# Kernel tuning notes

Measured on AMD Instinct MI355X. Metric: run time of the kernel, lower is better.

## Reference

```python
import jax, jax.numpy as jnp
import numpy as np

EPS = 1e-5  # InstanceNorm2d default eps


def setup_inputs() -> dict:
    key = jax.random.key(0)
    ks = jax.random.split(key, 6)
    B, S, C, KV, H = 4, 4096, 512, 960, 4
    emb = jax.random.normal(ks[0], (B, S, C), dtype=jnp.float32)
    emb_all = jax.random.normal(ks[1], (B, S, KV), dtype=jnp.float32)
    # nn.Linear weights are [out, in]; stacked per-head.
    Wq = jax.random.normal(ks[2], (H, C, C), dtype=jnp.float32) * 0.02
    Wk = jax.random.normal(ks[3], (H, KV, KV), dtype=jnp.float32) * 0.02
    Wv = jax.random.normal(ks[4], (H, KV, KV), dtype=jnp.float32) * 0.02
    Wo = jax.random.normal(ks[5], (C, C), dtype=jnp.float32) * 0.02
    return {"emb": emb, "emb_all": emb_all, "Wq": Wq, "Wk": Wk, "Wv": Wv, "Wo": Wo}


def reference(emb, emb_all, Wq, Wk, Wv, Wo):
    # Per-head linear projections (torch Linear: y = x @ W.T), batched over heads.
    Q = jnp.einsum('bsc,hdc->bhsd', emb, Wq)       # [B,H,S,C]
    K = jnp.einsum('bsk,hjk->bhsj', emb_all, Wk)   # [B,H,S,KV]
    V = jnp.einsum('bsk,hjk->bhsj', emb_all, Wv)   # [B,H,S,KV]
    kv_size = K.shape[-1]
    # Q is transposed(-1,-2) -> [B,H,C,S]; scores = Q^T @ K -> [B,H,C,KV]
    scores = jnp.einsum('bhsc,bhsk->bhck', Q, K) / jnp.sqrt(jnp.float32(kv_size))
    # InstanceNorm2d(num_heads): normalize each (b,h) plane over (C, KV), biased var, no affine.
    mean = jnp.mean(scores, axis=(2, 3), keepdims=True)
    var = jnp.var(scores, axis=(2, 3), keepdims=True)
    normed = (scores - mean) * jax.lax.rsqrt(var + EPS)
    probs = jax.nn.softmax(normed, axis=3)  # softmax over KV; dropout is identity (eval)
    # context = probs @ V^T -> [B,H,C,S]
    context = jnp.einsum('bhck,bhsk->bhcs', probs, V)
    # permute(0,3,2,1) -> [B,S,C,H], mean over heads -> [B,S,C]
    ctx = jnp.mean(context, axis=1).transpose(0, 2, 1)  # [B,S,C]
    out = jnp.einsum('bsc,dc->bsd', ctx, Wo)  # output Linear, no bias; proj dropout identity
    return out
```

## Files before the change

### kernel.cpp

```cpp
#include <hip/hip_runtime.h>
#include <math.h>

typedef __attribute__((ext_vector_type(8))) short short8;
typedef __attribute__((ext_vector_type(4))) float f32x4;

__device__ __forceinline__ unsigned short f2bf(float f) {
    unsigned int u; __builtin_memcpy(&u, &f, 4);
    unsigned int r = (u + 0x7FFFu + ((u >> 16) & 1u)) >> 16;
    return (unsigned short)r;
}
__device__ __forceinline__ float bf2f(unsigned short h) {
    unsigned int u = ((unsigned int)h) << 16;
    float f; __builtin_memcpy(&f, &u, 4); return f;
}
__device__ __forceinline__ void gl2lds16(const unsigned short* g, unsigned short* l) {
    __builtin_amdgcn_global_load_lds(
        (const __attribute__((address_space(1))) unsigned int*)g,
        (__attribute__((address_space(3))) unsigned int*)l, 16, 0, 0);
}

template<typename OutT, bool STATS>
__global__ __launch_bounds__(512)
void gemm_bt(const unsigned short* __restrict__ A, const unsigned short* __restrict__ B,
             OutT* __restrict__ C, float2* __restrict__ sp_out,
             int K, long lda, long ldb, long ldc,
             long sa_bb, long sa_bh, long sb_bb, long sb_bh, long sc_z,
             int H, float alpha)
{
    __shared__ unsigned short As[2][128 * 32];
    __shared__ unsigned short Bs[2][128 * 32];

    const int z = blockIdx.z;
    const int bb = z / H, hh = z - bb * H;
    A += (long)bb * sa_bb + (long)hh * sa_bh;
    B += (long)bb * sb_bb + (long)hh * sb_bh;
    C += (long)z * sc_z;

    const int tid  = threadIdx.x;
    const int lane = tid & 63;
    const int wave = tid >> 6;
    const int wr = wave >> 2, wc = wave & 3;

    const long m0 = (long)blockIdx.y * 128;
    const long n0 = (long)blockIdx.x * 128;

    const int lrow = lane >> 2;
    const int lcol = (lane & 3) * 8;
    const unsigned short* ga = A + (m0 + wave * 16 + lrow) * lda + lcol;
    const unsigned short* gb = B + (n0 + wave * 16 + lrow) * ldb + lcol;

    auto stg = [&](int buf, long koff) {
        gl2lds16(ga + koff, &As[buf][wave * 512]);
        gl2lds16(gb + koff, &Bs[buf][wave * 512]);
    };

    const int fr = lane & 15;
    const int fk = (lane >> 4) * 8;

    f32x4 acc[4][2];
    const f32x4 zero4 = {0.f, 0.f, 0.f, 0.f};
    #pragma unroll
    for (int i = 0; i < 4; ++i)
        #pragma unroll
        for (int j = 0; j < 2; ++j) acc[i][j] = zero4;

    stg(0, 0);
    stg(1, 32);

    int cur = 0;
    for (long k0 = 0; k0 < K; k0 += 32) {
        const bool ahead = (k0 + 64 < K);
        if (ahead) {
            asm volatile("s_waitcnt vmcnt(2)" ::: "memory");
        } else {
            asm volatile("s_waitcnt vmcnt(0)" ::: "memory");
        }
        __builtin_amdgcn_s_barrier();

        const unsigned short* ra = &As[cur][(wr * 64 + fr) * 32 + fk];
        const unsigned short* rb = &Bs[cur][(wc * 32 + fr) * 32 + fk];
        short8 af[4], bfr[2];
        #pragma unroll
        for (int i = 0; i < 4; ++i) af[i]  = *(const short8*)(ra + i * 512);
        #pragma unroll
        for (int j = 0; j < 2; ++j) bfr[j] = *(const short8*)(rb + j * 512);
        #pragma unroll
        for (int i = 0; i < 4; ++i)
            #pragma unroll
            for (int j = 0; j < 2; ++j)
                acc[i][j] = __builtin_amdgcn_mfma_f32_16x16x32_bf16(af[i], bfr[j], acc[i][j], 0, 0, 0);

        asm volatile("s_waitcnt lgkmcnt(0)" ::: "memory");
        __builtin_amdgcn_s_barrier();
        if (ahead) stg(cur, k0 + 64);
        cur ^= 1;
    }

    float s = 0.f, s2 = 0.f;
    const int orow = (lane >> 4) * 4;
    #pragma unroll
    for (int i = 0; i < 4; ++i) {
        const long rbase = m0 + wr * 64 + i * 16 + orow;
        #pragma unroll
        for (int j = 0; j < 2; ++j) {
            const long cidx = n0 + wc * 32 + j * 16 + fr;
            f32x4 v = acc[i][j];
            #pragma unroll
            for (int q = 0; q < 4; ++q) {
                float val = alpha * v[q];
                if constexpr (STATS) { s += val; s2 += val * val; }
                if constexpr (sizeof(OutT) == 4) C[(rbase + q) * ldc + cidx] = val;
                else                             C[(rbase + q) * ldc + cidx] = f2bf(val);
            }
        }
    }

    if constexpr (STATS) {
        float* red = (float*)&As[0][0];
        red[tid] = s; red[512 + tid] = s2;
        __syncthreads();
        for (int off = 256; off > 0; off >>= 1) {
            if (tid < off) { red[tid] += red[tid + off]; red[512 + tid] += red[512 + tid + off]; }
            __syncthreads();
        }
        if (tid == 0)
            sp_out[(long)z * 32 + blockIdx.y * gridDim.x + blockIdx.x] =
                make_float2(red[0], red[512]);
    }
}

__device__ __forceinline__
void tc64_impl(const float* __restrict__ in, unsigned short* __restrict__ outT,
               unsigned short* __restrict__ outB, int R, int Cin, long ldaT,
               int bx, int by, bool dual, unsigned short (*t)[68])
{
    const int r0 = bx * 64, c0 = by * 64;
    const int tid = threadIdx.x;
    const int rr  = tid >> 4;
    const int cc4 = (tid & 15) * 4;
    const bool real = (c0 + cc4) < Cin;

    #pragma unroll
    for (int i = 0; i < 4; ++i) {
        const int r = rr + i * 16;
        float4 v = make_float4(0.f, 0.f, 0.f, 0.f);
        if (real) v = *(const float4*)(in + (long)(r0 + r) * Cin + c0 + cc4);
        ushort4 o;
        o.x = f2bf(v.x); o.y = f2bf(v.y); o.z = f2bf(v.z); o.w = f2bf(v.w);
        *(ushort4*)&t[r][cc4] = o;
        if (dual && real)
            *(ushort4*)(outB + (long)(r0 + r) * Cin + c0 + cc4) = o;
    }
    __syncthreads();
    #pragma unroll
    for (int i = 0; i < 2; ++i) {
        const int p = rr + i * 16;
        const int c = 2 * p;
        ushort2 a0 = *(const ushort2*)&t[cc4 + 0][c];
        ushort2 a1 = *(const ushort2*)&t[cc4 + 1][c];
        ushort2 a2 = *(const ushort2*)&t[cc4 + 2][c];
        ushort2 a3 = *(const ushort2*)&t[cc4 + 3][c];
        ushort4 w0; w0.x = a0.x; w0.y = a1.x; w0.z = a2.x; w0.w = a3.x;
        ushort4 w1; w1.x = a0.y; w1.y = a1.y; w1.z = a2.y; w1.w = a3.y;
        *(ushort4*)(outT + (long)(c0 + c) * ldaT + r0 + cc4)     = w0;
        *(ushort4*)(outT + (long)(c0 + c + 1) * ldaT + r0 + cc4) = w1;
    }
}

__global__ __launch_bounds__(256)
void prep_all(const float* __restrict__ emb, const float* __restrict__ emb_all,
              const float* __restrict__ Wq, const float* __restrict__ Wk,
              const float* __restrict__ Wv, const float* __restrict__ Wo,
              unsigned short* __restrict__ embT, unsigned short* __restrict__ emb_allT,
              unsigned short* __restrict__ emb_allB, unsigned short* __restrict__ WqB,
              unsigned short* __restrict__ WkB, unsigned short* __restrict__ WvT,
              unsigned short* __restrict__ WoB)
{
    __shared__ unsigned short t[64][68];
    int bid = blockIdx.x;
    if (bid < 4096) {
        const int z = bid >> 10, r2 = bid & 1023, by = r2 >> 6, bx = r2 & 63;
        tc64_impl(emb_all + (long)z * 4096 * 960, emb_allT + (long)z * 1024 * 4096,
                  emb_allB + (long)z * 4096 * 960, 4096, 960, 4096, bx, by, true, t);
        return;
    }
    bid -= 4096;
    if (bid < 2048) {
        const int z = bid >> 9, r2 = bid & 511, by = r2 >> 6, bx = r2 & 63;
        tc64_impl(emb + (long)z * 4096 * 512, embT + (long)z * 512 * 4096,
                  nullptr, 4096, 512, 4096, bx, by, false, t);
        return;
    }
    bid -= 2048;
    if (bid < 960) {
        const int z = bid / 240, r2 = bid % 240, by = r2 / 15, bx = r2 % 15;
        tc64_impl(Wv + (long)z * 960 * 960, WvT + (long)z * 1024 * 960,
                  nullptr, 960, 960, 960, bx, by, false, t);
        return;
    }
    bid -= 960;
    long q = (long)bid * 256 + threadIdx.x;
    if (q < 983040) {
        long e = q * 4;
        long h = e / 983040L; long r2 = e - h * 983040L;
        long r = r2 / 960;    long c = r2 - r * 960;
        ushort4 o = {0, 0, 0, 0};
        if (r < 960) {
            float4 v = *(const float4*)(Wk + (h * 960 + r) * 960 + c);
            o.x = f2bf(v.x); o.y = f2bf(v.y); o.z = f2bf(v.z); o.w = f2bf(v.w);
        }
        *(ushort4*)(WkB + e) = o;
        return;
    }
    q -= 983040;
    if (q < 262144) {
        long e = q * 4;
        float4 v = *(const float4*)(Wq + e);
        ushort4 o; o.x = f2bf(v.x); o.y = f2bf(v.y); o.z = f2bf(v.z); o.w = f2bf(v.w);
        *(ushort4*)(WqB + e) = o;
        return;
    }
    q -= 262144;
    if (q < 65536) {
        long e = q * 4;
        float4 v = *(const float4*)(Wo + e);
        ushort4 o; o.x = f2bf(v.x); o.y = f2bf(v.y); o.z = f2bf(v.z); o.w = f2bf(v.w);
        *(ushort4*)(WoB + e) = o;
    }
}

__global__ __launch_bounds__(256)
void reduce_gt(const unsigned short* __restrict__ part, unsigned short* __restrict__ GT)
{
    long i = ((long)blockIdx.x * 256 + threadIdx.x) * 8;
    long b = i >> 19, r = i & 524287;
    const unsigned short* p = part + b * 4 * 524288 + r;
    const short8 v0 = *(const short8*)(p);
    const short8 v1 = *(const short8*)(p + 524288);
    const short8 v2 = *(const short8*)(p + 2 * 524288);
    const short8 v3 = *(const short8*)(p + 3 * 524288);
    short8 o;
    #pragma unroll
    for (int k = 0; k < 8; ++k) {
        float s = bf2f((unsigned short)v0[k]) + bf2f((unsigned short)v1[k])
                + bf2f((unsigned short)v2[k]) + bf2f((unsigned short)v3[k]);
        o[k] = (short)f2bf(s);
    }
    *(short8*)(GT + i) = o;
}

__global__ __launch_bounds__(256)
void norm_softmax(const unsigned short* __restrict__ SC, const float2* __restrict__ part,
                  unsigned short* __restrict__ probs)
{
    const int lane = threadIdx.x & 63;
    const int wave = threadIdx.x >> 6;
    const long row = (long)blockIdx.x * 4 + wave;
    const int z = (int)(row >> 9);

    float2 pv = part[z * 32 + (lane & 31)];
    float a = pv.x, b = pv.y;
    #pragma unroll
    for (int off = 1; off < 32; off <<= 1) {
        a += __shfl_xor(a, off);
        b += __shfl_xor(b, off);
    }
    const float ninv = 1.f / (512.f * 960.f);
    const float mean = a * ninv;
    const float rstd = rsqrtf(b * ninv - mean * mean + 960.f * 1e-5f);

    const unsigned short* p = SC + row * 1024 + lane * 16;
    const bool act = lane < 60;
    float x[16];
    {
        const short8 w0 = *(const short8*)(p);
        const short8 w1 = *(const short8*)(p + 8);
        #pragma unroll
        for (int k = 0; k < 8; ++k) {
            x[k]     = (bf2f((unsigned short)w0[k]) - mean) * rstd;
            x[k + 8] = (bf2f((unsigned short)w1[k]) - mean) * rstd;
        }
    }
    float mx = -1e30f;
    if (act) {
        #pragma unroll
        for (int k = 0; k < 16; ++k) mx = fmaxf(mx, x[k]);
    }
    #pragma unroll
    for (int off = 1; off < 64; off <<= 1) mx = fmaxf(mx, __shfl_xor(mx, off));

    float s = 0.f;
    if (act) {
        #pragma unroll
        for (int k = 0; k < 16; ++k) { x[k] = __expf(x[k] - mx); s += x[k]; }
    }
    #pragma unroll
    for (int off = 1; off < 64; off <<= 1) s += __shfl_xor(s, off);
    const float inv = 1.f / s;

    unsigned short* o = probs + row * 1024 + lane * 16;
    short8 o0 = {0,0,0,0,0,0,0,0}, o1 = {0,0,0,0,0,0,0,0};
    if (act) {
        #pragma unroll
        for (int k = 0; k < 8; ++k) {
            o0[k] = (short)f2bf(x[k] * inv);
            o1[k] = (short)f2bf(x[k + 8] * inv);
        }
    }
    *(short8*)(o)     = o0;
    *(short8*)(o + 8) = o1;
}

__global__ __launch_bounds__(256)
void mean_heads(const unsigned short* __restrict__ UT, unsigned short* __restrict__ Ub)
{
    const long per = 1024L * 512;
    long e = ((long)blockIdx.x * 256 + threadIdx.x) * 8;
    long b = e / per; long r = e - b * per;
    const short8 v0 = *(const short8*)(UT + (b * 4 + 0) * per + r);
    const short8 v1 = *(const short8*)(UT + (b * 4 + 1) * per + r);
    const short8 v2 = *(const short8*)(UT + (b * 4 + 2) * per + r);
    const short8 v3 = *(const short8*)(UT + (b * 4 + 3) * per + r);
    short8 o;
    #pragma unroll
    for (int k = 0; k < 8; ++k) {
        float s = bf2f((unsigned short)v0[k]) + bf2f((unsigned short)v1[k])
                + bf2f((unsigned short)v2[k]) + bf2f((unsigned short)v3[k]);
        o[k] = (short)f2bf(s);
    }
    *(short8*)(Ub + b * per + r) = o;
}

extern "C" void kernel_launch(void* const* d_in, const int* in_sizes, int n_in,
                              void* d_out, int out_size, void* d_ws, size_t ws_size,
                              hipStream_t stream)
{
    const float* emb     = (const float*)d_in[0];
    const float* emb_all = (const float*)d_in[1];
    const float* Wq      = (const float*)d_in[2];
    const float* Wk      = (const float*)d_in[3];
    const float* Wv      = (const float*)d_in[4];
    const float* Wo      = (const float*)d_in[5];
    float* out = (float*)d_out;

    char* ws = (char*)d_ws;
    unsigned short* embT     = (unsigned short*)(ws);
    unsigned short* emb_allT = (unsigned short*)(ws + 16777216);
    unsigned short* emb_allB = (unsigned short*)(ws + 50331648);
    unsigned short* WqB      = (unsigned short*)(ws + 81788928);
    unsigned short* WkB      = (unsigned short*)(ws + 83886080);
    unsigned short* WvT      = (unsigned short*)(ws + 91750400);
    unsigned short* WoB      = (unsigned short*)(ws + 99614720);
    unsigned short* GT       = (unsigned short*)(ws + 100139008);
    unsigned short* probs    = (unsigned short*)(ws + 104333312);
    float2* sc_part          = (float2*)(ws + 121110528);
    unsigned short* partK    = (unsigned short*)(ws + 134217728);

    unsigned short* S1  = embT;
    unsigned short* SC  = emb_allT;
    unsigned short* UT  = (unsigned short*)(ws + 33554432);
    unsigned short* UbT = GT;
    unsigned short* W2  = embT;

    prep_all<<<12224, 256, 0, stream>>>(emb, emb_all, Wq, Wk, Wv, Wo,
                                        embT, emb_allT, emb_allB, WqB, WkB, WvT, WoB);

    gemm_bt<unsigned short, false><<<dim3(4, 8, 16), 512, 0, stream>>>(
        emb_allT, embT, partK, nullptr, 1024, 4096, 4096, 512,
        1024L*4096, 1024, 512L*4096, 1024, 1024L*512, 4, 1.f);
    reduce_gt<<<1024, 256, 0, stream>>>(partK, GT);

    gemm_bt<unsigned short, false><<<dim3(8, 4, 16), 512, 0, stream>>>(
        WqB, GT, S1, nullptr, 512, 512, 512, 1024,
        0, 512L*512, 1024L*512, 0, 512L*1024, 4, 1.f);

    gemm_bt<unsigned short, true><<<dim3(8, 4, 16), 512, 0, stream>>>(
        S1, WkB, SC, sc_part, 960, 1024, 960, 1024,
        4L*512*1024, 512L*1024, 0, 1024L*960, 512L*1024, 4, 1.f);

    norm_softmax<<<2048, 256, 0, stream>>>(SC, sc_part, probs);

    gemm_bt<unsigned short, false><<<dim3(4, 8, 16), 512, 0, stream>>>(
        WvT, probs, UT, nullptr, 960, 960, 1024, 512,
        0, 1024L*960, 4L*512*1024, 512L*1024, 1024L*512, 4, 0.25f);

    mean_heads<<<1024, 256, 0, stream>>>(UT, UbT);

    gemm_bt<unsigned short, false><<<dim3(8, 4, 4), 512, 0, stream>>>(
        WoB, UbT, W2, nullptr, 512, 512, 512, 1024,
        0, 0, 1024L*512, 0, 512L*1024, 1, 1.f);

    gemm_bt<float, false><<<dim3(4, 32, 4), 512, 0, stream>>>(
        emb_allB, W2, out, nullptr, 960, 960, 1024, 512,
        4096L*960, 0, 512L*1024, 0, 4096L*512, 1, 1.f);
}
```

Before: 198.8 us.

## Deepen GEMM K-tile to 64 with XOR-swizzled LDS layout

Doubles the K depth of each staged tile from 32 to 64 so each barrier pair covers twice as many MFMAs, halving the loop and synchronisation overhead. Global-to-LDS copies now use an XOR swizzle on the 16-byte column chunk, and fragment reads apply the same swizzle to avoid LDS bank conflicts. It also adds a min-blocks-per-CU hint to launch bounds. LDS use per block doubles to 64 KB, which may limit occupancy, and the code assumes K is a multiple of 64.

```diff
diff --git a/kernel.cpp b/kernel.cpp
--- a/kernel.cpp
+++ b/kernel.cpp
@@ -20,15 +20,15 @@
 }
 
 template<typename OutT, bool STATS>
-__global__ __launch_bounds__(512)
+__global__ __launch_bounds__(512, 4)
 void gemm_bt(const unsigned short* __restrict__ A, const unsigned short* __restrict__ B,
              OutT* __restrict__ C, float2* __restrict__ sp_out,
              int K, long lda, long ldb, long ldc,
              long sa_bb, long sa_bh, long sb_bb, long sb_bh, long sc_z,
              int H, float alpha)
 {
-    __shared__ unsigned short As[2][128 * 32];
-    __shared__ unsigned short Bs[2][128 * 32];
+    __shared__ unsigned short As[2][128 * 64];
+    __shared__ unsigned short Bs[2][128 * 64];
 
     const int z = blockIdx.z;
     const int bb = z / H, hh = z - bb * H;
@@ -44,18 +44,23 @@
     const long m0 = (long)blockIdx.y * 128;
     const long n0 = (long)blockIdx.x * 128;
 
-    const int lrow = lane >> 2;
-    const int lcol = (lane & 3) * 8;
-    const unsigned short* ga = A + (m0 + wave * 16 + lrow) * lda + lcol;
-    const unsigned short* gb = B + (n0 + wave * 16 + lrow) * ldb + lcol;
+    const int lrow = lane >> 3;
+    const int kc   = ((lane & 7) ^ (lrow & 7)) * 8;
+    const unsigned short* ga0 = A + (m0 + wave * 16 + lrow) * lda + kc;
+    const unsigned short* ga1 = ga0 + 8 * lda;
+    const unsigned short* gb0 = B + (n0 + wave * 16 + lrow) * ldb + kc;
+    const unsigned short* gb1 = gb0 + 8 * ldb;
 
     auto stg = [&](int buf, long koff) {
-        gl2lds16(ga + koff, &As[buf][wave * 512]);
-        gl2lds16(gb + koff, &Bs[buf][wave * 512]);
+        gl2lds16(ga0 + koff, &As[buf][wave * 1024]);
+        gl2lds16(ga1 + koff, &As[buf][wave * 1024 + 512]);
+        gl2lds16(gb0 + koff, &Bs[buf][wave * 1024]);
+        gl2lds16(gb1 + koff, &Bs[buf][wave * 1024 + 512]);
     };
 
     const int fr = lane & 15;
-    const int fk = (lane >> 4) * 8;
+    const int hi = lane >> 4;
+    const int sw = fr & 7;
 
     f32x4 acc[4][2];
     const f32x4 zero4 = {0.f, 0.f, 0.f, 0.f};
@@ -65,39 +70,45 @@
         for (int j = 0; j < 2; ++j) acc[i][j] = zero4;
 
     stg(0, 0);
-    stg(1, 32);
+    stg(1, 64);
 
     int cur = 0;
-    for (long k0 = 0; k0 < K; k0 += 32) {
-        const bool ahead = (k0 + 64 < K);
-        if (ahead) {
-            asm volatile("s_waitcnt vmcnt(2)" ::: "memory");
+    for (long k0 = 0; k0 < K; k0 += 64) {
+        if (k0 + 64 < K) {
+            asm volatile("s_waitcnt vmcnt(4)" ::: "memory");
         } else {
             asm volatile("s_waitcnt vmcnt(0)" ::: "memory");
         }
         __builtin_amdgcn_s_barrier();
 
-        const unsigned short* ra = &As[cur][(wr * 64 + fr) * 32 + fk];
-        const unsigned short* rb = &Bs[cur][(wc * 32 + fr) * 32 + fk];
-        short8 af[4], bfr[2];
-        #pragma unroll
-        for (int i = 0; i < 4; ++i) af[i]  = *(const short8*)(ra + i * 512);
-        #pragma unroll
-        for (int j = 0; j < 2; ++j) bfr[j] = *(const short8*)(rb + j * 512);
-        #pragma unroll
-        for (int i = 0; i < 4; ++i)
+        #pragma unroll
+        for (int kk = 0; kk < 2; ++kk) {
+            short8 af[4], bfr[2];
             #pragma unroll
-            for (int j = 0; j < 2; ++j)
-                acc[i][j] = __builtin_amdgcn_mfma_f32_16x16x32_bf16(af[i], bfr[j], acc[i][j], 0, 0, 0);
+            for (int i = 0; i < 4; ++i) {
+                const int row = wr * 64 + i * 16 + fr;
+                af[i] = *(const short8*)(&As[cur][row * 64 + (((kk * 4 + hi) ^ sw) * 8)]);
+            }
+            #pragma unroll
+            for (int j = 0; j < 2; ++j) {
+                const int row = wc * 32 + j * 16 + fr;
+                bfr[j] = *(const short8*)(&Bs[cur][row * 64 + (((kk * 4 + hi) ^ sw) * 8)]);
+            }
+            #pragma unroll
+            for (int i = 0; i < 4; ++i)
+                #pragma unroll
+                for (int j = 0; j < 2; ++j)
+                    acc[i][j] = __builtin_amdgcn_mfma_f32_16x16x32_bf16(af[i], bfr[j], acc[i][j], 0, 0, 0);
+        }
 
         asm volatile("s_waitcnt lgkmcnt(0)" ::: "memory");
         __builtin_amdgcn_s_barrier();
-        if (ahead) stg(cur, k0 + 64);
+        if (k0 + 128 < K) stg(cur, k0 + 128);
         cur ^= 1;
     }
 
     float s = 0.f, s2 = 0.f;
-    const int orow = (lane >> 4) * 4;
+    const int orow = hi * 4;
     #pragma unroll
     for (int i = 0; i < 4; ++i) {
         const long rbase = m0 + wr * 64 + i * 16 + orow;
```

Result: faster. 186.8 us, median of 2 (-6.0%).
